# Kernel tuning notes

Measured on AMD Instinct MI355X. Metric: run time of the kernel, lower is better.

The kernel has to match this reference:

```python
import jax, jax.numpy as jnp
import numpy as np

S = 8192      # s: number of persons/nodes
F = 1024      # feature_len
A = 256       # attn_len
SIGMA_X, SIGMA_Y = 4.0, 1.0
EPS_VALID = 1e-8
EPS_DIS = 1e-4


def setup_inputs() -> dict:
    key = jax.random.key(0)
    ks = jax.random.split(key, 8)
    batch_data = jax.random.normal(ks[0], (S, F), dtype=jnp.float32)
    xywh = jax.random.uniform(ks[1], (S, 4), dtype=jnp.float32)  # positive -> all rows valid
    actor_weights = jax.random.uniform(ks[2], (S,), dtype=jnp.float32)
    avg_pos = jax.random.uniform(ks[3], (S, 2), dtype=jnp.float32)
    # learned params (kaiming-ish init, zero bias as in original)
    W_h = jax.random.normal(ks[4], (F, 2), dtype=jnp.float32) * (2.0 / F) ** 0.5
    b_h = jnp.zeros((2,), dtype=jnp.float32)
    W_g = jax.random.normal(ks[5], (F, A), dtype=jnp.float32) * (2.0 / F) ** 0.5
    b_g = jnp.zeros((A,), dtype=jnp.float32)
    return {
        "batch_data": batch_data, "xywh": xywh, "OW": 1920, "OH": 1080,
        "actor_weights": actor_weights, "avg_pos": avg_pos,
        "W_h": W_h, "b_h": b_h, "W_g": W_g, "b_g": b_g, "num_person": S,
    }


def reference(batch_data, xywh, OW, OH, actor_weights, avg_pos, W_h, b_h, W_g, b_g, num_person):
    # highlight_fc + tanh -> predicted offsets [S,2]
    hp = jnp.tanh(batch_data @ W_h + b_h)
    hx = hp[:, 0] * xywh[:, 2] * SIGMA_X + xywh[:, 0]  # [S]
    hy = hp[:, 1] * xywh[:, 3] * SIGMA_Y + xywh[:, 1]  # [S]

    # gcn_fc + relu -> node messages [S,A]
    targets = jax.nn.relu(batch_data @ W_g + b_g)

    # valid rows/cols: torch loop skips i/j with sum(xywh) < 1e-8
    valid = jnp.sum(xywh, axis=1) >= EPS_VALID  # [S] bool

    # pairwise inverse-distance weights [S,S] (the memory-bound core)
    dx = hx[:, None] - xywh[None, :, 0]
    dy = hy[:, None] - xywh[None, :, 1]
    dis = jnp.sqrt(dx * dx + dy * dy)
    pair_valid = valid[:, None] & valid[None, :]
    w = jnp.where(pair_valid, 1.0 / (dis + EPS_DIS), 0.0)
    row_sum = jnp.sum(w, axis=1, keepdims=True)
    w = jnp.where(valid[:, None], w / jnp.maximum(row_sum, 1e-30), 0.0)

    targets_weighted = w @ targets  # [S,A]
    return (targets_weighted, hp)
```

## Files before the change

kernel.cpp:

```cpp
#include <hip/hip_runtime.h>
#include <math.h>
#include <stdint.h>

typedef __attribute__((ext_vector_type(8))) short short8;
typedef __attribute__((ext_vector_type(4))) float f32x4;

__device__ __forceinline__ uint32_t cvt_pk_bf16(float lo, float hi) {
  uint32_t r;
  asm("v_cvt_pk_bf16_f32 %0, %1, %2" : "=v"(r) : "v"(lo), "v"(hi));
  return r;
}

__device__ __forceinline__ float wfun(float hx, float hy, float cx, float cy) {
  float dx = hx - cx, dy = hy - cy;
  float d = __builtin_amdgcn_sqrtf(fmaf(dx, dx, dy * dy));
  return __builtin_amdgcn_rcpf(d + 1e-4f);
}

__global__ __launch_bounds__(256) void k_head(
    const float* __restrict__ batch, const float* __restrict__ xywh,
    const float* __restrict__ W_h, const float* __restrict__ b_h,
    float* __restrict__ hp_out, float* __restrict__ hx, float* __restrict__ hy,
    float* __restrict__ validf, float2* __restrict__ cxy, int S, int F) {
  int wid = threadIdx.x >> 6;
  int lane = threadIdx.x & 63;
  int row = blockIdx.x * 4 + wid;
  if (row >= S) return;
  const float4* brow = (const float4*)(batch + (size_t)row * F);
  const float4* wh4 = (const float4*)W_h;
  int nf4 = F >> 2;
  float acc0 = 0.f, acc1 = 0.f;
  for (int k4 = lane; k4 < nf4; k4 += 64) {
    float4 b = brow[k4];
    float4 wa = wh4[2 * k4];
    float4 wb = wh4[2 * k4 + 1];
    acc0 += b.x * wa.x + b.y * wa.z + b.z * wb.x + b.w * wb.z;
    acc1 += b.x * wa.y + b.y * wa.w + b.z * wb.y + b.w * wb.w;
  }
  #pragma unroll
  for (int off = 32; off; off >>= 1) {
    acc0 += __shfl_xor(acc0, off, 64);
    acc1 += __shfl_xor(acc1, off, 64);
  }
  if (lane == 0) {
    float hp0 = tanhf(acc0 + b_h[0]);
    float hp1 = tanhf(acc1 + b_h[1]);
    float4 xy = ((const float4*)xywh)[row];
    hp_out[2 * row] = hp0;
    hp_out[2 * row + 1] = hp1;
    hx[row] = hp0 * xy.z * 4.0f + xy.x;
    hy[row] = hp1 * xy.w * 1.0f + xy.y;
    bool v = (xy.x + xy.y + xy.z + xy.w >= 1e-8f);
    validf[row] = v ? 1.0f : 0.0f;
    cxy[row] = v ? make_float2(xy.x, xy.y) : make_float2(1e30f, 1e30f);
  }
}

__global__ __launch_bounds__(256) void k_prep_w(
    const float* __restrict__ Wg, uint16_t* __restrict__ WgT, int F, int A) {
  int idx = blockIdx.x * 256 + threadIdx.x;
  int a = idx % A;
  int k0 = (idx / A) * 8;
  if (k0 >= F) return;
  float f[8];
  #pragma unroll
  for (int e = 0; e < 8; ++e) f[e] = Wg[(size_t)(k0 + e) * A + a];
  uint4 v;
  v.x = cvt_pk_bf16(f[0], f[1]);
  v.y = cvt_pk_bf16(f[2], f[3]);
  v.z = cvt_pk_bf16(f[4], f[5]);
  v.w = cvt_pk_bf16(f[6], f[7]);
  *(uint4*)(WgT + (size_t)a * F + k0) = v;
}

__global__ __launch_bounds__(256) void k_targets_mfma(
    const float* __restrict__ batch, const uint16_t* __restrict__ WgT,
    const float* __restrict__ bg, uint16_t* __restrict__ tgt2,
    int S, int F, int A) {
  int t = threadIdx.x;
  int lane = t & 63, wid = t >> 6;
  int wm = wid >> 1, wn = wid & 1;
  int i0 = blockIdx.x * 32;
  int row = i0 + wm * 16 + (lane & 15);
  int kch = lane >> 4;
  const float* ab = batch + (size_t)row * F + kch * 8;
  int ncol0 = wn * 128 + (lane & 15);
  const uint16_t* bb = WgT + (size_t)ncol0 * F + kch * 8;

  f32x4 acc[8] = {};
  float4 a0 = *(const float4*)(ab);
  float4 a1 = *(const float4*)(ab + 4);
  short8 bf[8];
  #pragma unroll
  for (int nf = 0; nf < 8; ++nf)
    bf[nf] = *(const short8*)(bb + (size_t)nf * 16 * F);

  for (int k0 = 0; k0 < F; k0 += 32) {
    int kn = (k0 + 32 < F) ? k0 + 32 : 0;
    float4 na0 = *(const float4*)(ab + kn);
    float4 na1 = *(const float4*)(ab + kn + 4);
    short8 nbf[8];
    #pragma unroll
    for (int nf = 0; nf < 8; ++nf)
      nbf[nf] = *(const short8*)(bb + kn + (size_t)nf * 16 * F);
    union { short8 s; uint32_t u[4]; } af;
    af.u[0] = cvt_pk_bf16(a0.x, a0.y);
    af.u[1] = cvt_pk_bf16(a0.z, a0.w);
    af.u[2] = cvt_pk_bf16(a1.x, a1.y);
    af.u[3] = cvt_pk_bf16(a1.z, a1.w);
    #pragma unroll
    for (int nf = 0; nf < 8; ++nf)
      acc[nf] = __builtin_amdgcn_mfma_f32_16x16x32_bf16(af.s, bf[nf], acc[nf], 0, 0, 0);
    a0 = na0; a1 = na1;
    #pragma unroll
    for (int nf = 0; nf < 8; ++nf) bf[nf] = nbf[nf];
  }

  int jb = blockIdx.x;
  int rloc = wm * 16 + (lane >> 4) * 4;
  #pragma unroll
  for (int nf = 0; nf < 8; ++nf) {
    int col = ncol0 + nf * 16;
    float b = bg[col];
    float o0 = fmaxf(acc[nf][0] + b, 0.f);
    float o1 = fmaxf(acc[nf][1] + b, 0.f);
    float o2 = fmaxf(acc[nf][2] + b, 0.f);
    float o3 = fmaxf(acc[nf][3] + b, 0.f);
    uint2 pk;
    pk.x = cvt_pk_bf16(o0, o1);
    pk.y = cvt_pk_bf16(o2, o3);
    *(uint2*)(tgt2 + ((size_t)jb * A + col) * 32 + rloc) = pk;
  }
}

__global__ __launch_bounds__(1024, 4) void k_gather_v16(
    const uint16_t* __restrict__ tgt2, const float2* __restrict__ cxy,
    const float* __restrict__ hx, const float* __restrict__ hy,
    const float* __restrict__ validf, float* __restrict__ out, int S, int A) {
  __shared__ uint16_t Bt[2][2][256][40];
  __shared__ uint32_t Af[2][2][2][64][4];
  __shared__ float comb[32][260];
  __shared__ float rs_l[2][32][16];
  __shared__ float scale_s[32];

  int t = threadIdx.x;
  int lane = t & 63, wid = t >> 6;
  int kg = wid >> 3;
  int sub = wid & 7;
  int wm = sub >> 2, wn = sub & 3;
  int i0 = blockIdx.x * 32;
  int kch = lane >> 4;
  int n0 = wn * 64 + (lane & 15);
  int NT = (S >> 1) / 32;
  const size_t TSTRIDE = (size_t)A * 32;
  const int COLS = 40;

  int u = t & 511;
  int wr = u & 31;
  int wjp = u >> 5;
  float hx_w = hx[i0 + wr], hy_w = hy[i0 + wr];
  uint32_t* afw0 = &Af[0][kg][wr >> 4][(wr & 15) | ((wjp >> 2) << 4)][wjp & 3];
  uint32_t* afw1 = &Af[1][kg][wr >> 4][(wr & 15) | ((wjp >> 2) << 4)][wjp & 3];
  const float2* gC = cxy + (size_t)kg * (S >> 1) + 2 * wjp;

  int scol = u >> 1;
  int skw = u & 1;
  const uint16_t* gB0 = tgt2 + (size_t)(kg * NT) * TSTRIDE
                        + (size_t)scol * 32 + skw * 16;

  f32x4 acc[4] = {};
  float rs = 0.f;

  {
    float4 c0 = *(const float4*)(gC);
    float wA = wfun(hx_w, hy_w, c0.x, c0.y);
    float wB = wfun(hx_w, hy_w, c0.z, c0.w);
    rs += wA + wB;
    *afw0 = cvt_pk_bf16(wA, wB);
    uint4 ga = *(const uint4*)(gB0);
    uint4 gb = *(const uint4*)(gB0 + 8);
    *(uint4*)&Bt[0][kg][scol][skw * 16] = ga;
    *(uint4*)&Bt[0][kg][scol][skw * 16 + 8] = gb;
  }
  float4 ccur = *(const float4*)(gC + 32);
  __syncthreads();

  for (int ts = 0; ts < NT; ++ts) {
    int nxt = (ts & 1) ^ 1;
    int tn = (ts + 1 < NT) ? ts + 1 : 0;
    int tf = (ts + 2 < NT) ? ts + 2 : 0;

    const uint16_t* bp = gB0 + (size_t)tn * TSTRIDE;
    uint4 ga = *(const uint4*)(bp);
    uint4 gb = *(const uint4*)(bp + 8);
    float4 cfut = *(const float4*)(gC + (size_t)tf * 32);

    const uint32_t* afp = &Af[ts & 1][kg][wm][lane][0];
    short8 afr = *(const short8*)afp;
    const uint16_t* br = &Bt[ts & 1][kg][n0][kch * 8];
    short8 b0 = *(const short8*)(br);
    short8 b1 = *(const short8*)(br + 16 * COLS);
    short8 b2 = *(const short8*)(br + 32 * COLS);
    short8 b3 = *(const short8*)(br + 48 * COLS);

    acc[0] = __builtin_amdgcn_mfma_f32_16x16x32_bf16(afr, b0, acc[0], 0, 0, 0);
    acc[1] = __builtin_amdgcn_mfma_f32_16x16x32_bf16(afr, b1, acc[1], 0, 0, 0);
    acc[2] = __builtin_amdgcn_mfma_f32_16x16x32_bf16(afr, b2, acc[2], 0, 0, 0);
    acc[3] = __builtin_amdgcn_mfma_f32_16x16x32_bf16(afr, b3, acc[3], 0, 0, 0);

    float wA = wfun(hx_w, hy_w, ccur.x, ccur.y);
    float wB = wfun(hx_w, hy_w, ccur.z, ccur.w);
    float g = (ts + 1 < NT) ? 1.f : 0.f;
    rs = fmaf(g, wA + wB, rs);
    uint32_t pk = cvt_pk_bf16(wA, wB);
    uint32_t* afw = nxt ? afw1 : afw0;
    *afw = pk;

    *(uint4*)&Bt[nxt][kg][scol][skw * 16] = ga;
    *(uint4*)&Bt[nxt][kg][scol][skw * 16 + 8] = gb;
    ccur = cfut;
    __syncthreads();
  }

  rs_l[kg][wr][wjp] = rs;

  if (kg == 1) {
    int mre = wm * 16 + (lane >> 4) * 4;
    #pragma unroll
    for (int r = 0; r < 4; ++r) {
      comb[mre + r][n0]      = acc[0][r];
      comb[mre + r][n0 + 16] = acc[1][r];
      comb[mre + r][n0 + 32] = acc[2][r];
      comb[mre + r][n0 + 48] = acc[3][r];
    }
  }
  __syncthreads();
  if (t < 32) {
    float r = 0.f;
    #pragma unroll
    for (int jp = 0; jp < 16; ++jp) r += rs_l[0][t][jp] + rs_l[1][t][jp];
    float v = validf[i0 + t];
    scale_s[t] = (v > 0.f) ? 1.0f / fmaxf(r, 1e-30f) : 0.f;
  }
  __syncthreads();
  if (kg == 0) {
    int mre = wm * 16 + (lane >> 4) * 4;
    #pragma unroll
    for (int r = 0; r < 4; ++r) {
      float s = scale_s[mre + r];
      size_t base = (size_t)(i0 + mre + r) * A;
      out[base + n0]      = (acc[0][r] + comb[mre + r][n0]) * s;
      out[base + n0 + 16] = (acc[1][r] + comb[mre + r][n0 + 16]) * s;
      out[base + n0 + 32] = (acc[2][r] + comb[mre + r][n0 + 32]) * s;
      out[base + n0 + 48] = (acc[3][r] + comb[mre + r][n0 + 48]) * s;
    }
  }
}

extern "C" void kernel_launch(void* const* d_in, const int* in_sizes, int n_in,
                              void* d_out, int out_size, void* d_ws, size_t ws_size,
                              hipStream_t stream) {
  const float* batch = (const float*)d_in[0];
  const float* xywh  = (const float*)d_in[1];
  const float* W_h   = (const float*)d_in[6];
  const float* b_h   = (const float*)d_in[7];
  const float* W_g   = (const float*)d_in[8];
  const float* b_g   = (const float*)d_in[9];
  int S = in_sizes[4];
  int F = in_sizes[0] / S;
  int A = in_sizes[9];

  float* out    = (float*)d_out;
  float* out_tw = out;
  float* out_hp = out + (size_t)S * A;

  uint16_t* tgt2 = (uint16_t*)d_ws;
  uint16_t* WgT  = tgt2 + (size_t)A * S;
  float* hxv = (float*)(WgT + (size_t)A * F);
  float* hyv = hxv + S;
  float* vfv = hyv + S;
  float2* cxyv = (float2*)(vfv + S);

  k_head<<<dim3((S + 3) / 4), 256, 0, stream>>>(batch, xywh, W_h, b_h,
                                                out_hp, hxv, hyv, vfv, cxyv, S, F);
  k_prep_w<<<dim3((A * F / 8 + 255) / 256), 256, 0, stream>>>(W_g, WgT, F, A);
  k_targets_mfma<<<dim3(S / 32), 256, 0, stream>>>(batch, WgT, b_g, tgt2, S, F, A);
  k_gather_v16<<<dim3(S / 32), 1024, 0, stream>>>(tgt2, cxyv, hxv, hyv, vfv,
                                                  out_tw, S, A);
}
```

Measured before the change: 145.6 us.

## Split gather K four ways with single-buffered tiles and 2D targets grid

The gather kernel now splits the S reduction across four wave groups instead of two. Each wave computes both 16-row halves, so one B fragment feeds two MFMAs. Tile staging moves from a double buffer to a single buffer guarded by two barriers per step, and each thread loads a full 32-element column. The partial accumulators are combined through shared memory in three rounds. The targets GEMM launches a 2D grid over column halves, doubling block count and halving per-thread accumulators to improve occupancy. The extra barriers and combine rounds add synchronisation cost.

```diff
diff --git a/kernel.cpp b/kernel.cpp
--- a/kernel.cpp
+++ b/kernel.cpp
@@ -80,28 +80,28 @@
   int t = threadIdx.x;
   int lane = t & 63, wid = t >> 6;
   int wm = wid >> 1, wn = wid & 1;
-  int i0 = blockIdx.x * 32;
+  int i0 = blockIdx.y * 32;
   int row = i0 + wm * 16 + (lane & 15);
   int kch = lane >> 4;
   const float* ab = batch + (size_t)row * F + kch * 8;
-  int ncol0 = wn * 128 + (lane & 15);
+  int ncol0 = blockIdx.x * 128 + wn * 64 + (lane & 15);
   const uint16_t* bb = WgT + (size_t)ncol0 * F + kch * 8;
 
-  f32x4 acc[8] = {};
+  f32x4 acc[4] = {};
   float4 a0 = *(const float4*)(ab);
   float4 a1 = *(const float4*)(ab + 4);
-  short8 bf[8];
-  #pragma unroll
-  for (int nf = 0; nf < 8; ++nf)
+  short8 bf[4];
+  #pragma unroll
+  for (int nf = 0; nf < 4; ++nf)
     bf[nf] = *(const short8*)(bb + (size_t)nf * 16 * F);
 
   for (int k0 = 0; k0 < F; k0 += 32) {
     int kn = (k0 + 32 < F) ? k0 + 32 : 0;
     float4 na0 = *(const float4*)(ab + kn);
     float4 na1 = *(const float4*)(ab + kn + 4);
-    short8 nbf[8];
-    #pragma unroll
-    for (int nf = 0; nf < 8; ++nf)
+    short8 nbf[4];
+    #pragma unroll
+    for (int nf = 0; nf < 4; ++nf)
       nbf[nf] = *(const short8*)(bb + kn + (size_t)nf * 16 * F);
     union { short8 s; uint32_t u[4]; } af;
     af.u[0] = cvt_pk_bf16(a0.x, a0.y);
@@ -109,17 +109,17 @@
     af.u[2] = cvt_pk_bf16(a1.x, a1.y);
     af.u[3] = cvt_pk_bf16(a1.z, a1.w);
     #pragma unroll
-    for (int nf = 0; nf < 8; ++nf)
+    for (int nf = 0; nf < 4; ++nf)
       acc[nf] = __builtin_amdgcn_mfma_f32_16x16x32_bf16(af.s, bf[nf], acc[nf], 0, 0, 0);
     a0 = na0; a1 = na1;
     #pragma unroll
-    for (int nf = 0; nf < 8; ++nf) bf[nf] = nbf[nf];
-  }
-
-  int jb = blockIdx.x;
+    for (int nf = 0; nf < 4; ++nf) bf[nf] = nbf[nf];
+  }
+
+  int jb = blockIdx.y;
   int rloc = wm * 16 + (lane >> 4) * 4;
   #pragma unroll
-  for (int nf = 0; nf < 8; ++nf) {
+  for (int nf = 0; nf < 4; ++nf) {
     int col = ncol0 + nf * 16;
     float b = bg[col];
     float o0 = fmaxf(acc[nf][0] + b, 0.f);
@@ -133,126 +133,182 @@
   }
 }
 
-__global__ __launch_bounds__(1024, 4) void k_gather_v16(
+__global__ __launch_bounds__(1024, 4) void k_gather_v17(
     const uint16_t* __restrict__ tgt2, const float2* __restrict__ cxy,
     const float* __restrict__ hx, const float* __restrict__ hy,
     const float* __restrict__ validf, float* __restrict__ out, int S, int A) {
-  __shared__ uint16_t Bt[2][2][256][40];
-  __shared__ uint32_t Af[2][2][2][64][4];
+  __shared__ uint16_t Bt[4][256][40];
+  __shared__ uint32_t Af[4][2][64][4];
   __shared__ float comb[32][260];
-  __shared__ float rs_l[2][32][16];
+  __shared__ float rs_l[4][32][8];
   __shared__ float scale_s[32];
 
   int t = threadIdx.x;
   int lane = t & 63, wid = t >> 6;
-  int kg = wid >> 3;
-  int sub = wid & 7;
-  int wm = sub >> 2, wn = sub & 3;
+  int kg = wid >> 2;
+  int wn = wid & 3;
   int i0 = blockIdx.x * 32;
   int kch = lane >> 4;
   int n0 = wn * 64 + (lane & 15);
-  int NT = (S >> 1) / 32;
+  int NT = S / (4 * 32);
   const size_t TSTRIDE = (size_t)A * 32;
-  const int COLS = 40;
-
-  int u = t & 511;
-  int wr = u & 31;
-  int wjp = u >> 5;
+
+  int wkg = t >> 8;
+  int v = t & 255;
+  int wr = v & 31;
+  int wjp8 = v >> 5;
   float hx_w = hx[i0 + wr], hy_w = hy[i0 + wr];
-  uint32_t* afw0 = &Af[0][kg][wr >> 4][(wr & 15) | ((wjp >> 2) << 4)][wjp & 3];
-  uint32_t* afw1 = &Af[1][kg][wr >> 4][(wr & 15) | ((wjp >> 2) << 4)][wjp & 3];
-  const float2* gC = cxy + (size_t)kg * (S >> 1) + 2 * wjp;
-
-  int scol = u >> 1;
-  int skw = u & 1;
-  const uint16_t* gB0 = tgt2 + (size_t)(kg * NT) * TSTRIDE
-                        + (size_t)scol * 32 + skw * 16;
-
-  f32x4 acc[4] = {};
+  int rgw = wr >> 4;
+  int L0 = (wr & 15) | ((wjp8 >> 2) << 4);
+  int L1 = (wr & 15) | (((wjp8 >> 2) + 2) << 4);
+  int sl = wjp8 & 3;
+  const float2* gCp = cxy + (size_t)wkg * (S >> 2) + 2 * wjp8;
+
+  int scol = v;
+  const uint16_t* gB0 = tgt2 + (size_t)(wkg * NT) * TSTRIDE + (size_t)scol * 32;
+
+  f32x4 acc0[4] = {};
+  f32x4 acc1[4] = {};
   float rs = 0.f;
 
   {
-    float4 c0 = *(const float4*)(gC);
-    float wA = wfun(hx_w, hy_w, c0.x, c0.y);
-    float wB = wfun(hx_w, hy_w, c0.z, c0.w);
-    rs += wA + wB;
-    *afw0 = cvt_pk_bf16(wA, wB);
-    uint4 ga = *(const uint4*)(gB0);
-    uint4 gb = *(const uint4*)(gB0 + 8);
-    *(uint4*)&Bt[0][kg][scol][skw * 16] = ga;
-    *(uint4*)&Bt[0][kg][scol][skw * 16 + 8] = gb;
-  }
-  float4 ccur = *(const float4*)(gC + 32);
+    uint4 q0 = *(const uint4*)(gB0);
+    uint4 q1 = *(const uint4*)(gB0 + 8);
+    uint4 q2 = *(const uint4*)(gB0 + 16);
+    uint4 q3 = *(const uint4*)(gB0 + 24);
+    *(uint4*)&Bt[wkg][scol][0]  = q0;
+    *(uint4*)&Bt[wkg][scol][8]  = q1;
+    *(uint4*)&Bt[wkg][scol][16] = q2;
+    *(uint4*)&Bt[wkg][scol][24] = q3;
+    float4 ca = *(const float4*)(gCp);
+    float4 cb = *(const float4*)(gCp + 16);
+    float wA = wfun(hx_w, hy_w, ca.x, ca.y);
+    float wB = wfun(hx_w, hy_w, ca.z, ca.w);
+    float wC = wfun(hx_w, hy_w, cb.x, cb.y);
+    float wD = wfun(hx_w, hy_w, cb.z, cb.w);
+    rs += (wA + wB) + (wC + wD);
+    Af[wkg][rgw][L0][sl] = cvt_pk_bf16(wA, wB);
+    Af[wkg][rgw][L1][sl] = cvt_pk_bf16(wC, wD);
+  }
   __syncthreads();
+  float4 ccur0 = *(const float4*)(gCp + 32);
+  float4 ccur1 = *(const float4*)(gCp + 48);
 
   for (int ts = 0; ts < NT; ++ts) {
-    int nxt = (ts & 1) ^ 1;
     int tn = (ts + 1 < NT) ? ts + 1 : 0;
     int tf = (ts + 2 < NT) ? ts + 2 : 0;
 
     const uint16_t* bp = gB0 + (size_t)tn * TSTRIDE;
-    uint4 ga = *(const uint4*)(bp);
-    uint4 gb = *(const uint4*)(bp + 8);
-    float4 cfut = *(const float4*)(gC + (size_t)tf * 32);
-
-    const uint32_t* afp = &Af[ts & 1][kg][wm][lane][0];
-    short8 afr = *(const short8*)afp;
-    const uint16_t* br = &Bt[ts & 1][kg][n0][kch * 8];
+    uint4 q0 = *(const uint4*)(bp);
+    uint4 q1 = *(const uint4*)(bp + 8);
+    uint4 q2 = *(const uint4*)(bp + 16);
+    uint4 q3 = *(const uint4*)(bp + 24);
+    float4 cf0 = *(const float4*)(gCp + (size_t)tf * 32);
+    float4 cf1 = *(const float4*)(gCp + (size_t)tf * 32 + 16);
+
+    short8 a0 = *(const short8*)&Af[kg][0][lane][0];
+    short8 a1 = *(const short8*)&Af[kg][1][lane][0];
+    const uint16_t* br = &Bt[kg][n0][kch * 8];
     short8 b0 = *(const short8*)(br);
-    short8 b1 = *(const short8*)(br + 16 * COLS);
-    short8 b2 = *(const short8*)(br + 32 * COLS);
-    short8 b3 = *(const short8*)(br + 48 * COLS);
-
-    acc[0] = __builtin_amdgcn_mfma_f32_16x16x32_bf16(afr, b0, acc[0], 0, 0, 0);
-    acc[1] = __builtin_amdgcn_mfma_f32_16x16x32_bf16(afr, b1, acc[1], 0, 0, 0);
-    acc[2] = __builtin_amdgcn_mfma_f32_16x16x32_bf16(afr, b2, acc[2], 0, 0, 0);
-    acc[3] = __builtin_amdgcn_mfma_f32_16x16x32_bf16(afr, b3, acc[3], 0, 0, 0);
-
-    float wA = wfun(hx_w, hy_w, ccur.x, ccur.y);
-    float wB = wfun(hx_w, hy_w, ccur.z, ccur.w);
+    short8 b1 = *(const short8*)(br + 16 * 40);
+    short8 b2 = *(const short8*)(br + 32 * 40);
+    short8 b3 = *(const short8*)(br + 48 * 40);
+
+    acc0[0] = __builtin_amdgcn_mfma_f32_16x16x32_bf16(a0, b0, acc0[0], 0, 0, 0);
+    acc0[1] = __builtin_amdgcn_mfma_f32_16x16x32_bf16(a0, b1, acc0[1], 0, 0, 0);
+    acc0[2] = __builtin_amdgcn_mfma_f32_16x16x32_bf16(a0, b2, acc0[2], 0, 0, 0);
+    acc0[3] = __builtin_amdgcn_mfma_f32_16x16x32_bf16(a0, b3, acc0[3], 0, 0, 0);
+    acc1[0] = __builtin_amdgcn_mfma_f32_16x16x32_bf16(a1, b0, acc1[0], 0, 0, 0);
+    acc1[1] = __builtin_amdgcn_mfma_f32_16x16x32_bf16(a1, b1, acc1[1], 0, 0, 0);
+    acc1[2] = __builtin_amdgcn_mfma_f32_16x16x32_bf16(a1, b2, acc1[2], 0, 0, 0);
+    acc1[3] = __builtin_amdgcn_mfma_f32_16x16x32_bf16(a1, b3, acc1[3], 0, 0, 0);
+
+    float wA = wfun(hx_w, hy_w, ccur0.x, ccur0.y);
+    float wB = wfun(hx_w, hy_w, ccur0.z, ccur0.w);
+    float wC = wfun(hx_w, hy_w, ccur1.x, ccur1.y);
+    float wD = wfun(hx_w, hy_w, ccur1.z, ccur1.w);
     float g = (ts + 1 < NT) ? 1.f : 0.f;
-    rs = fmaf(g, wA + wB, rs);
-    uint32_t pk = cvt_pk_bf16(wA, wB);
-    uint32_t* afw = nxt ? afw1 : afw0;
-    *afw = pk;
-
-    *(uint4*)&Bt[nxt][kg][scol][skw * 16] = ga;
-    *(uint4*)&Bt[nxt][kg][scol][skw * 16 + 8] = gb;
-    ccur = cfut;
+    rs = fmaf(g, (wA + wB) + (wC + wD), rs);
+    uint32_t pkA = cvt_pk_bf16(wA, wB);
+    uint32_t pkB = cvt_pk_bf16(wC, wD);
+
     __syncthreads();
-  }
-
-  rs_l[kg][wr][wjp] = rs;
-
-  if (kg == 1) {
-    int mre = wm * 16 + (lane >> 4) * 4;
-    #pragma unroll
-    for (int r = 0; r < 4; ++r) {
-      comb[mre + r][n0]      = acc[0][r];
-      comb[mre + r][n0 + 16] = acc[1][r];
-      comb[mre + r][n0 + 32] = acc[2][r];
-      comb[mre + r][n0 + 48] = acc[3][r];
-    }
-  }
+
+    *(uint4*)&Bt[wkg][scol][0]  = q0;
+    *(uint4*)&Bt[wkg][scol][8]  = q1;
+    *(uint4*)&Bt[wkg][scol][16] = q2;
+    *(uint4*)&Bt[wkg][scol][24] = q3;
+    Af[wkg][rgw][L0][sl] = pkA;
+    Af[wkg][rgw][L1][sl] = pkB;
+
+    __syncthreads();
+    ccur0 = cf0;
+    ccur1 = cf1;
+  }
+
+  rs_l[wkg][wr][wjp8] = rs;
   __syncthreads();
   if (t < 32) {
     float r = 0.f;
     #pragma unroll
-    for (int jp = 0; jp < 16; ++jp) r += rs_l[0][t][jp] + rs_l[1][t][jp];
-    float v = validf[i0 + t];
-    scale_s[t] = (v > 0.f) ? 1.0f / fmaxf(r, 1e-30f) : 0.f;
+    for (int k = 0; k < 4; ++k)
+      #pragma unroll
+      for (int jp = 0; jp < 8; ++jp) r += rs_l[k][t][jp];
+    float fv = validf[i0 + t];
+    scale_s[t] = (fv > 0.f) ? 1.0f / fmaxf(r, 1e-30f) : 0.f;
   }
   __syncthreads();
+
+  int rbase = (lane >> 4) * 4;
+  #pragma unroll
+  for (int round = 1; round < 4; ++round) {
+    if (kg == round) {
+      #pragma unroll
+      for (int r = 0; r < 4; ++r) {
+        comb[rbase + r][n0]      = acc0[0][r];
+        comb[rbase + r][n0 + 16] = acc0[1][r];
+        comb[rbase + r][n0 + 32] = acc0[2][r];
+        comb[rbase + r][n0 + 48] = acc0[3][r];
+        comb[16 + rbase + r][n0]      = acc1[0][r];
+        comb[16 + rbase + r][n0 + 16] = acc1[1][r];
+        comb[16 + rbase + r][n0 + 32] = acc1[2][r];
+        comb[16 + rbase + r][n0 + 48] = acc1[3][r];
+      }
+    }
+    __syncthreads();
+    if (kg == 0) {
+      #pragma unroll
+      for (int r = 0; r < 4; ++r) {
+        acc0[0][r] += comb[rbase + r][n0];
+        acc0[1][r] += comb[rbase + r][n0 + 16];
+        acc0[2][r] += comb[rbase + r][n0 + 32];
+        acc0[3][r] += comb[rbase + r][n0 + 48];
+        acc1[0][r] += comb[16 + rbase + r][n0];
+        acc1[1][r] += comb[16 + rbase + r][n0 + 16];
+        acc1[2][r] += comb[16 + rbase + r][n0 + 32];
+        acc1[3][r] += comb[16 + rbase + r][n0 + 48];
+      }
+    }
+    __syncthreads();
+  }
+
   if (kg == 0) {
-    int mre = wm * 16 + (lane >> 4) * 4;
     #pragma unroll
     for (int r = 0; r < 4; ++r) {
-      float s = scale_s[mre + r];
-      size_t base = (size_t)(i0 + mre + r) * A;
-      out[base + n0]      = (acc[0][r] + comb[mre + r][n0]) * s;
-      out[base + n0 + 16] = (acc[1][r] + comb[mre + r][n0 + 16]) * s;
-      out[base + n0 + 32] = (acc[2][r] + comb[mre + r][n0 + 32]) * s;
-      out[base + n0 + 48] = (acc[3][r] + comb[mre + r][n0 + 48]) * s;
+      int row0 = rbase + r;
+      float s0 = scale_s[row0];
+      size_t base0 = (size_t)(i0 + row0) * A;
+      out[base0 + n0]      = acc0[0][r] * s0;
+      out[base0 + n0 + 16] = acc0[1][r] * s0;
+      out[base0 + n0 + 32] = acc0[2][r] * s0;
+      out[base0 + n0 + 48] = acc0[3][r] * s0;
+      int row1 = 16 + rbase + r;
+      float s1 = scale_s[row1];
+      size_t base1 = (size_t)(i0 + row1) * A;
+      out[base1 + n0]      = acc1[0][r] * s1;
+      out[base1 + n0 + 16] = acc1[1][r] * s1;
+      out[base1 + n0 + 32] = acc1[2][r] * s1;
+      out[base1 + n0 + 48] = acc1[3][r] * s1;
     }
   }
 }
@@ -284,7 +340,8 @@
   k_head<<<dim3((S + 3) / 4), 256, 0, stream>>>(batch, xywh, W_h, b_h,
                                                 out_hp, hxv, hyv, vfv, cxyv, S, F);
   k_prep_w<<<dim3((A * F / 8 + 255) / 256), 256, 0, stream>>>(W_g, WgT, F, A);
-  k_targets_mfma<<<dim3(S / 32), 256, 0, stream>>>(batch, WgT, b_g, tgt2, S, F, A);
-  k_gather_v16<<<dim3(S / 32), 1024, 0, stream>>>(tgt2, cxyv, hxv, hyv, vfv,
+  k_targets_mfma<<<dim3(A / 128, S / 32), 256, 0, stream>>>(batch, WgT, b_g,
+                                                            tgt2, S, F, A);
+  k_gather_v17<<<dim3(S / 32), 1024, 0, stream>>>(tgt2, cxyv, hxv, hyv, vfv,
                                                   out_tw, S, A);
 }
```

After: 155.9 us. 1.07x slower.
